# Optimization experiments

Measured on AMD Instinct MI355X. Metric: run time of the kernel, lower is better.

Reference implementation:

```python
import jax, jax.numpy as jnp
import numpy as np

N_SEQ, N_RES, C_M = 512, 256, 256
C_OUTER, C_Z = 32, 128
LN_EPS = 1e-5
NORM_EPS = 1e-3


def setup_inputs() -> dict:
    key = jax.random.key(0)
    ks = jax.random.split(key, 6)
    f32 = jnp.float32
    return {
        "act": jax.random.normal(ks[0], (N_SEQ, N_RES, C_M), f32),
        "mask": jnp.ones((N_SEQ, N_RES), f32),
        # LayerNorm params (create_scale=True, create_offset=True)
        "ln_scale": jnp.ones((C_M,), f32),
        "ln_offset": jnp.zeros((C_M,), f32),
        # left/right projections, 'linear' (VarianceScaling fan_in scale=1)
        "left_w": (jax.random.normal(ks[1], (C_M, C_OUTER), f32) / np.float32(np.sqrt(C_M))),
        "left_b": jnp.zeros((C_OUTER,), f32),
        "right_w": (jax.random.normal(ks[2], (C_M, C_OUTER), f32) / np.float32(np.sqrt(C_M))),
        "right_b": jnp.zeros((C_OUTER,), f32),
        # output_w: VarianceScaling(scale=2.0, fan_in) over (c_outer, c_outer) input dims
        "output_w": (jax.random.normal(ks[3], (C_OUTER, C_OUTER, C_Z), f32)
                     * np.float32(np.sqrt(2.0 / (C_OUTER * C_OUTER)))),
        "output_b": jnp.zeros((C_Z,), f32),
    }


def reference(act, mask, ln_scale, ln_offset, left_w, left_b, right_w, right_b,
              output_w, output_b):
    # LayerNorm over last axis
    mu = jnp.mean(act, axis=-1, keepdims=True)
    var = jnp.var(act, axis=-1, keepdims=True)
    x = (act - mu) * jax.lax.rsqrt(var + LN_EPS) * ln_scale + ln_offset

    m = mask[..., None]  # [N_seq, N_res, 1]
    left = m * (jnp.einsum('abm,mc->abc', x, left_w) + left_b)    # [A,B,Co]
    right = m * (jnp.einsum('abm,me->abe', x, right_w) + right_b)  # [A,D,Co]

    # mean outer product: sum over MSA depth a -> [B, D, Co, Co]
    op = jnp.einsum('abc,ade->bdce', left, right)
    out = jnp.einsum('bdce,cef->bdf', op, output_w) + output_b  # [B, D, Cz]

    # normalization by pairwise mask counts
    norm = jnp.einsum('ab,ad->bd', mask, mask)[..., None]  # [B, D, 1]
    return out / (NORM_EPS + norm)
```

## Files before the change

### kernel.cpp

```cpp
#include <hip/hip_runtime.h>
#include <hip/hip_bf16.h>
#include <stdint.h>

typedef short bf16x8 __attribute__((ext_vector_type(8)));
typedef float f32x4 __attribute__((ext_vector_type(4)));
typedef float f32x16 __attribute__((ext_vector_type(16)));
typedef unsigned short u16x4 __attribute__((ext_vector_type(4)));
typedef unsigned short u16x8 __attribute__((ext_vector_type(8)));

#define GLOAD16(g, l) __builtin_amdgcn_global_load_lds( \
    (const __attribute__((address_space(1))) void*)(g), \
    (__attribute__((address_space(3))) void*)(l), 16, 0, 0)

__device__ __forceinline__ unsigned short f2bf(float f) {
  unsigned u = __float_as_uint(f);
  unsigned r = (u + 0x7fffu + ((u >> 16) & 1u)) >> 16;
  return (unsigned short)r;
}

__global__ __launch_bounds__(256) void prep_norm_k(
    const float* __restrict__ lw, const float* __restrict__ rw,
    const float* __restrict__ ow, const float* __restrict__ mask,
    unsigned short* __restrict__ Wt, unsigned short* __restrict__ wfragG,
    float* __restrict__ nrm) {
  const int bid = blockIdx.x;
  if (bid < 512) {
    int idx = bid * 256 + threadIdx.x;
    if (idx < 131072) {
      int f = idx >> 10, k2 = idx & 1023;
      int e = k2 >> 5, c = k2 & 31;
      Wt[idx] = f2bf(ow[(size_t)((c << 5) + e) * 128 + f]);
    }
    if (idx < 16384) {
      int frag = idx >> 9, lane = (idx >> 3) & 63, j = idx & 7;
      int wc = frag >> 4, ni = (frag >> 3) & 1, kk = frag & 7;
      int mrow = lane & 15, g = lane >> 4;
      int c = wc * 32 + ni * 16 + mrow;
      int k = kk * 32 + g * 8 + j;
      wfragG[idx] = f2bf(c < 32 ? lw[k * 32 + c] : rw[k * 32 + (c - 32)]);
    }
  } else {
    const int b = bid - 512, d = threadIdx.x;
    float s = 0.f;
    #pragma unroll 8
    for (int a = 0; a < 512; ++a)
      s += mask[a * 256 + b] * mask[a * 256 + d];
    nrm[(b << 8) + d] = s;
  }
}

__global__ __launch_bounds__(256, 4) void ln_proj(
    const float* __restrict__ act, const float* __restrict__ mask,
    const float* __restrict__ lns, const float* __restrict__ lno,
    const float* __restrict__ lb, const float* __restrict__ rb,
    const unsigned short* __restrict__ wfragG,
    unsigned short* __restrict__ Lt, unsigned short* __restrict__ Rt) {
  __shared__ char smem[32768];
  const int tid = threadIdx.x;
  const int lane = tid & 63;
  const int w = tid >> 6;
  const int b = blockIdx.y;
  const int a0 = blockIdx.x << 6;
  const int l = tid & 15;
  const int rg = tid >> 4;

  f32x4 sc[4], of[4];
  #pragma unroll
  for (int j = 0; j < 4; ++j) {
    sc[j] = *(const f32x4*)(lns + (l << 4) + (j << 2));
    of[j] = *(const f32x4*)(lno + (l << 4) + (j << 2));
  }

  #pragma unroll
  for (int i = 0; i < 4; ++i) {
    const int r = rg + (i << 4);
    const float* src = act + ((size_t)(a0 + r) * 256 + b) * 256 + (l << 4);
    f32x4 xv[4];
    #pragma unroll
    for (int j = 0; j < 4; ++j) xv[j] = *(const f32x4*)(src + (j << 2));
    float s = 0.f, sq = 0.f;
    #pragma unroll
    for (int j = 0; j < 4; ++j) {
      f32x4 v = xv[j];
      s += v[0] + v[1] + v[2] + v[3];
      sq += v[0] * v[0] + v[1] * v[1] + v[2] * v[2] + v[3] * v[3];
    }
    s += __shfl_xor(s, 1); sq += __shfl_xor(sq, 1);
    s += __shfl_xor(s, 2); sq += __shfl_xor(sq, 2);
    s += __shfl_xor(s, 4); sq += __shfl_xor(sq, 4);
    s += __shfl_xor(s, 8); sq += __shfl_xor(sq, 8);
    const float mu = s * (1.f / 256.f);
    const float rs = rsqrtf(sq * (1.f / 256.f) - mu * mu + 1e-5f);
    #pragma unroll
    for (int hh = 0; hh < 2; ++hh) {
      u16x8 pk;
      #pragma unroll
      for (int j2 = 0; j2 < 2; ++j2) {
        const int j = (hh << 1) + j2;
        #pragma unroll
        for (int e = 0; e < 4; ++e)
          pk[(j2 << 2) + e] = f2bf((xv[j][e] - mu) * rs * sc[j][e] + of[j][e]);
      }
      const int c = (l << 1) + hh;
      *(u16x8*)(smem + (r << 9) + ((c ^ (r & 7)) << 4)) = pk;
    }
  }
  __syncthreads();

  const int wr = w >> 1, wc = w & 1;
  const int mrow = lane & 15, g = lane >> 4;
  f32x4 acc[2][2];
  #pragma unroll
  for (int i = 0; i < 2; ++i)
    #pragma unroll
    for (int jj = 0; jj < 2; ++jj) acc[i][jj] = (f32x4){0.f, 0.f, 0.f, 0.f};
  #pragma unroll
  for (int kk = 0; kk < 8; ++kk) {
    bf16x8 af[2], bfr[2];
    #pragma unroll
    for (int mi = 0; mi < 2; ++mi) {
      const int row = (wr << 5) + (mi << 4) + mrow;
      af[mi] = *(const bf16x8*)(smem + (row << 9) + ((((kk << 2) + g) ^ (row & 7)) << 4));
    }
    #pragma unroll
    for (int ni = 0; ni < 2; ++ni)
      bfr[ni] = *(const bf16x8*)(wfragG + (size_t)((((wc << 1) + ni) << 3) + kk) * 512 + (lane << 3));
    #pragma unroll
    for (int mi = 0; mi < 2; ++mi)
      #pragma unroll
      for (int ni = 0; ni < 2; ++ni)
        acc[mi][ni] = __builtin_amdgcn_mfma_f32_16x16x32_bf16(af[mi], bfr[ni], acc[mi][ni], 0, 0, 0);
  }
  __syncthreads();

  #pragma unroll
  for (int ni = 0; ni < 2; ++ni) {
    const int c = (wc << 5) + (ni << 4) + mrow;
    const float bias = (wc == 0) ? lb[(ni << 4) + mrow] : rb[(ni << 4) + mrow];
    #pragma unroll
    for (int mi = 0; mi < 2; ++mi) {
      const int aB = (wr << 5) + (mi << 4) + (g << 2);
      u16x4 pk;
      #pragma unroll
      for (int qq = 0; qq < 4; ++qq) {
        const float mk = mask[(size_t)(a0 + aB + qq) * 256 + b];
        pk[qq] = f2bf((acc[mi][ni][qq] + bias) * mk);
      }
      *(u16x4*)(smem + (c << 7) + ((((aB >> 3) & 7) ^ (c & 7)) << 4) + ((aB & 7) << 1)) = pk;
    }
  }
  __syncthreads();

  #pragma unroll
  for (int s = 0; s < 2; ++s) {
    const int c = (w << 4) + (s << 3) + (lane >> 3);
    const int gr = lane & 7;
    const u16x8 v = *(const u16x8*)(smem + (c << 7) + ((gr ^ (c & 7)) << 4));
    unsigned short* dst = (c < 32) ? Lt : Rt;
    *(u16x8*)(dst + (size_t)(b * 32 + (c & 31)) * 512 + a0 + (gr << 3)) = v;
  }
}

__global__ __launch_bounds__(512, 2) void gemm_fused(
    const unsigned short* __restrict__ Lt, const unsigned short* __restrict__ Rt,
    const unsigned short* __restrict__ Wt, const float* __restrict__ nrm,
    const float* __restrict__ outb, float* __restrict__ out) {
  __shared__ char smem[131072];
  const int tid = threadIdx.x;
  const int lane = tid & 63;
  const int w = tid >> 6;
  const int wr = w >> 2, wc = w & 3;
  const int l31 = lane & 31, hi = lane >> 5;
  const int mrow = lane & 15, g = lane >> 4;

  const int bid = blockIdx.x;
  const int xcd = bid & 7, jj_ = bid >> 3;
  const int mb = ((jj_ >> 5) << 3) | (jj_ & 7);
  const int nb = (xcd << 2) | ((jj_ >> 3) & 3);
  const int m0i = mb << 8, n0i = nb << 8;

  const int scol = (((tid & 7) ^ ((tid >> 3) & 7)) << 3);

  f32x16 acc32[4][2];
  #pragma unroll
  for (int i = 0; i < 4; ++i)
    #pragma unroll
    for (int jj = 0; jj < 2; ++jj)
      #pragma unroll
      for (int e = 0; e < 16; ++e) acc32[i][jj][e] = 0.f;

  auto STG = [&](const unsigned short* gsrc, int baserow, int dstoff, int kt) {
    GLOAD16(gsrc + ((size_t)(baserow + (tid >> 3)) << 9) + (kt << 6) + scol,
            smem + dstoff + (tid << 4));
  };
  auto STGALL = [&](int buf, int kt) {
    STG(Rt, n0i, buf + 32768, kt);        STG(Rt, n0i + 64, buf + 40960, kt);
    STG(Rt, n0i + 128, buf + 49152, kt);  STG(Rt, n0i + 192, buf + 57344, kt);
    STG(Lt, m0i, buf + 0, kt);            STG(Lt, m0i + 64, buf + 8192, kt);
    STG(Lt, m0i + 128, buf + 16384, kt);  STG(Lt, m0i + 192, buf + 24576, kt);
  };

  STGALL(0, 0);
  STGALL(65536, 1);
  asm volatile("s_waitcnt vmcnt(8)" ::: "memory");
  __builtin_amdgcn_s_barrier();

  #pragma unroll 1
  for (int t = 0; t < 8; ++t) {
    const char* bufp = smem + ((t & 1) << 16);
    #pragma unroll
    for (int kk = 0; kk < 4; ++kk) {
      bf16x8 af[4], bfv[2];
      #pragma unroll
      for (int Mg = 0; Mg < 4; ++Mg) {
        const int row = (wr << 7) + (Mg << 5) + l31;
        af[Mg] = *(const bf16x8*)(bufp + (row << 7) +
                                  ((((kk << 1) + hi) ^ (row & 7)) << 4));
      }
      #pragma unroll
      for (int Ng = 0; Ng < 2; ++Ng) {
        const int row = (wc << 6) + (Ng << 5) + l31;
        bfv[Ng] = *(const bf16x8*)(bufp + 32768 + (row << 7) +
                                   ((((kk << 1) + hi) ^ (row & 7)) << 4));
      }
      #pragma unroll
      for (int Mg = 0; Mg < 4; ++Mg)
        #pragma unroll
        for (int Ng = 0; Ng < 2; ++Ng)
          acc32[Mg][Ng] = __builtin_amdgcn_mfma_f32_32x32x16_bf16(
              af[Mg], bfv[Ng], acc32[Mg][Ng], 0, 0, 0);
    }
    if (t < 6) {
      __builtin_amdgcn_s_barrier();
      STGALL((t & 1) << 16, t + 2);
      asm volatile("s_waitcnt vmcnt(8)" ::: "memory");
      __builtin_amdgcn_s_barrier();
    } else if (t == 6) {
      asm volatile("s_waitcnt vmcnt(0)" ::: "memory");
      __builtin_amdgcn_s_barrier();
    }
  }
  __syncthreads();

  #pragma unroll
  for (int Mg = 0; Mg < 4; ++Mg) {
    #pragma unroll
    for (int Ng = 0; Ng < 2; ++Ng) {
      const int p = (((wr << 2) + Mg) << 3) | ((wc << 1) + Ng);
      #pragma unroll
      for (int q = 0; q < 4; ++q) {
        const int c0 = (q << 3) + (hi << 2);
        const int ow_ = (l31 << 6) + (c0 << 1);
        u16x4 pk;
        #pragma unroll
        for (int j = 0; j < 4; ++j) pk[j] = f2bf(acc32[Mg][Ng][(q << 2) + j]);
        *(u16x4*)(smem + (p << 11) +
                  (ow_ ^ ((p & 7) << 4) ^ (((ow_ >> 7) & 7) << 4))) = pk;
      }
    }
  }
  __syncthreads();

  f32x4 invn[4];
  #pragma unroll
  for (int pg = 0; pg < 4; ++pg) {
    const int bb = (mb << 3) + (pg << 1) + (g >> 1);
    const f32x4 nv = *(const f32x4*)(nrm + (bb << 8) + (nb << 3) + ((g & 1) << 2));
    #pragma unroll
    for (int qq = 0; qq < 4; ++qq) invn[pg][qq] = __builtin_amdgcn_rcpf(1e-3f + nv[qq]);
  }

  const int f0 = w << 4;
  f32x4 acc2[4];
  #pragma unroll
  for (int i = 0; i < 4; ++i) acc2[i] = (f32x4){0.f, 0.f, 0.f, 0.f};
  const unsigned short* wrow = Wt + (size_t)(f0 + mrow) * 1024;
  #pragma unroll 8
  for (int kk2 = 0; kk2 < 32; ++kk2) {
    const bf16x8 b2 = *(const bf16x8*)(wrow + (kk2 << 5) + (g << 3));
    const int orr = (kk2 << 6) + (g << 4);
    #pragma unroll
    for (int pg = 0; pg < 4; ++pg) {
      const int prow = (pg << 4) + mrow;
      const bf16x8 a2 = *(const bf16x8*)(smem + (prow << 11) +
          (orr ^ ((prow & 7) << 4) ^ (((orr >> 7) & 7) << 4)));
      acc2[pg] = __builtin_amdgcn_mfma_f32_16x16x32_bf16(a2, b2, acc2[pg], 0, 0, 0);
    }
  }

  const float ob_ = outb[f0 + mrow];
  #pragma unroll
  for (int pg = 0; pg < 4; ++pg) {
    #pragma unroll
    for (int qq = 0; qq < 4; ++qq) {
      const int p = (pg << 4) + (g << 2) + qq;
      const int bb = (mb << 3) + (p >> 3);
      const int dd = (nb << 3) + (p & 7);
      out[(size_t)((bb << 8) + dd) * 128 + f0 + mrow] = (acc2[pg][qq] + ob_) * invn[pg][qq];
    }
  }
}

extern "C" void kernel_launch(void* const* d_in, const int* in_sizes, int n_in,
                              void* d_out, int out_size, void* d_ws, size_t ws_size,
                              hipStream_t stream) {
  const float* act = (const float*)d_in[0];
  const float* mask = (const float*)d_in[1];
  const float* lns = (const float*)d_in[2];
  const float* lno = (const float*)d_in[3];
  const float* lw = (const float*)d_in[4];
  const float* lb = (const float*)d_in[5];
  const float* rw = (const float*)d_in[6];
  const float* rbv = (const float*)d_in[7];
  const float* ow = (const float*)d_in[8];
  const float* ob = (const float*)d_in[9];
  float* out = (float*)d_out;
  char* ws = (char*)d_ws;

  unsigned short* Lt = (unsigned short*)(ws);
  unsigned short* Rt = (unsigned short*)(ws + 8388608);
  unsigned short* Wt = (unsigned short*)(ws + 16777216);
  unsigned short* wfragG = (unsigned short*)(ws + 17039360);
  float* nrm = (float*)(ws + 17072128);

  hipLaunchKernelGGL(prep_norm_k, dim3(768), dim3(256), 0, stream,
                     lw, rw, ow, mask, Wt, wfragG, nrm);
  hipLaunchKernelGGL(ln_proj, dim3(8, 256), dim3(256), 0, stream,
                     act, mask, lns, lno, lb, rbv, wfragG, Lt, Rt);
  hipLaunchKernelGGL(gemm_fused, dim3(1024), dim3(512), 0, stream,
                     Lt, Rt, Wt, nrm, ob, out);
}
```

Before: 156.7 us.

## Shrink outer-product GEMM tile to 256x128 with triple-buffered 32-wide K pipeline

Rewrites the fused outer-product GEMM to use 256x128 output tiles and 16x16x32 MFMAs instead of 256x256 tiles with 32x32x16 MFMAs. The K loop now runs 16 steps of 32 through a three-stage LDS ring with one barrier per step, and it raises MFMA priority around the compute block. Halving LDS use (73 KB) and accumulator registers lets the kernel target 4 waves per SIMD and launch twice as many blocks, aiming for better latency hiding and load balance. In exchange, A/B reuse per tile drops and global traffic for L rows rises, and the smaller 16x16 MFMAs issue more instructions per FLOP.

```diff
diff --git a/kernel.cpp b/kernel.cpp
--- a/kernel.cpp
+++ b/kernel.cpp
@@ -4,7 +4,6 @@
 
 typedef short bf16x8 __attribute__((ext_vector_type(8)));
 typedef float f32x4 __attribute__((ext_vector_type(4)));
-typedef float f32x16 __attribute__((ext_vector_type(16)));
 typedef unsigned short u16x4 __attribute__((ext_vector_type(4)));
 typedef unsigned short u16x8 __attribute__((ext_vector_type(8)));
 
@@ -161,126 +160,117 @@
   }
 }
 
-__global__ __launch_bounds__(512, 2) void gemm_fused(
+__global__ __launch_bounds__(512, 4) void gemm_fused(
     const unsigned short* __restrict__ Lt, const unsigned short* __restrict__ Rt,
     const unsigned short* __restrict__ Wt, const float* __restrict__ nrm,
     const float* __restrict__ outb, float* __restrict__ out) {
-  __shared__ char smem[131072];
+  __shared__ char smem[73728];
   const int tid = threadIdx.x;
   const int lane = tid & 63;
   const int w = tid >> 6;
-  const int wr = w >> 2, wc = w & 3;
-  const int l31 = lane & 31, hi = lane >> 5;
+  const int wr = w >> 1, wn = w & 1;
   const int mrow = lane & 15, g = lane >> 4;
 
   const int bid = blockIdx.x;
-  const int xcd = bid & 7, jj_ = bid >> 3;
-  const int mb = ((jj_ >> 5) << 3) | (jj_ & 7);
-  const int nb = (xcd << 2) | ((jj_ >> 3) & 3);
-  const int m0i = mb << 8, n0i = nb << 8;
-
-  const int scol = (((tid & 7) ^ ((tid >> 3) & 7)) << 3);
-
-  f32x16 acc32[4][2];
+  const int xcd = bid & 7, j = bid >> 3;
+  const int sub = j & 63;
+  const int mb = ((j >> 6) << 3) + (sub >> 3);
+  const int nb = (xcd << 3) + (sub & 7);
+  const int m0i = mb << 8, n0i = nb << 7;
+
+  const int srow = tid >> 2;
+  const int scol = (((tid & 3) ^ (srow & 3)) << 3);
+
+  f32x4 acc[4][4];
   #pragma unroll
   for (int i = 0; i < 4; ++i)
     #pragma unroll
-    for (int jj = 0; jj < 2; ++jj)
-      #pragma unroll
-      for (int e = 0; e < 16; ++e) acc32[i][jj][e] = 0.f;
-
-  auto STG = [&](const unsigned short* gsrc, int baserow, int dstoff, int kt) {
-    GLOAD16(gsrc + ((size_t)(baserow + (tid >> 3)) << 9) + (kt << 6) + scol,
-            smem + dstoff + (tid << 4));
+    for (int jj = 0; jj < 4; ++jj) acc[i][jj] = (f32x4){0.f, 0.f, 0.f, 0.f};
+
+  auto STGA = [&](int buf, int half, int kt) {
+    GLOAD16(Lt + ((size_t)(m0i + (half << 7) + srow) << 9) + (kt << 5) + scol,
+            smem + buf + (half << 13) + (tid << 4));
   };
-  auto STGALL = [&](int buf, int kt) {
-    STG(Rt, n0i, buf + 32768, kt);        STG(Rt, n0i + 64, buf + 40960, kt);
-    STG(Rt, n0i + 128, buf + 49152, kt);  STG(Rt, n0i + 192, buf + 57344, kt);
-    STG(Lt, m0i, buf + 0, kt);            STG(Lt, m0i + 64, buf + 8192, kt);
-    STG(Lt, m0i + 128, buf + 16384, kt);  STG(Lt, m0i + 192, buf + 24576, kt);
+  auto STGB = [&](int buf, int kt) {
+    GLOAD16(Rt + ((size_t)(n0i + srow) << 9) + (kt << 5) + scol,
+            smem + buf + 16384 + (tid << 4));
   };
 
-  STGALL(0, 0);
-  STGALL(65536, 1);
-  asm volatile("s_waitcnt vmcnt(8)" ::: "memory");
+  STGA(0, 0, 0); STGA(0, 1, 0); STGB(0, 0);
+  STGA(24576, 0, 1); STGA(24576, 1, 1); STGB(24576, 1);
+  asm volatile("s_waitcnt vmcnt(3)" ::: "memory");
   __builtin_amdgcn_s_barrier();
 
+  int cur = 0;
   #pragma unroll 1
-  for (int t = 0; t < 8; ++t) {
-    const char* bufp = smem + ((t & 1) << 16);
-    #pragma unroll
-    for (int kk = 0; kk < 4; ++kk) {
-      bf16x8 af[4], bfv[2];
-      #pragma unroll
-      for (int Mg = 0; Mg < 4; ++Mg) {
-        const int row = (wr << 7) + (Mg << 5) + l31;
-        af[Mg] = *(const bf16x8*)(bufp + (row << 7) +
-                                  ((((kk << 1) + hi) ^ (row & 7)) << 4));
-      }
-      #pragma unroll
-      for (int Ng = 0; Ng < 2; ++Ng) {
-        const int row = (wc << 6) + (Ng << 5) + l31;
-        bfv[Ng] = *(const bf16x8*)(bufp + 32768 + (row << 7) +
-                                   ((((kk << 1) + hi) ^ (row & 7)) << 4));
-      }
-      #pragma unroll
-      for (int Mg = 0; Mg < 4; ++Mg)
-        #pragma unroll
-        for (int Ng = 0; Ng < 2; ++Ng)
-          acc32[Mg][Ng] = __builtin_amdgcn_mfma_f32_32x32x16_bf16(
-              af[Mg], bfv[Ng], acc32[Mg][Ng], 0, 0, 0);
-    }
-    if (t < 6) {
-      __builtin_amdgcn_s_barrier();
-      STGALL((t & 1) << 16, t + 2);
-      asm volatile("s_waitcnt vmcnt(8)" ::: "memory");
-      __builtin_amdgcn_s_barrier();
-    } else if (t == 6) {
-      asm volatile("s_waitcnt vmcnt(0)" ::: "memory");
-      __builtin_amdgcn_s_barrier();
-    }
-  }
-  __syncthreads();
-
-  #pragma unroll
-  for (int Mg = 0; Mg < 4; ++Mg) {
-    #pragma unroll
-    for (int Ng = 0; Ng < 2; ++Ng) {
-      const int p = (((wr << 2) + Mg) << 3) | ((wc << 1) + Ng);
-      #pragma unroll
-      for (int q = 0; q < 4; ++q) {
-        const int c0 = (q << 3) + (hi << 2);
-        const int ow_ = (l31 << 6) + (c0 << 1);
-        u16x4 pk;
-        #pragma unroll
-        for (int j = 0; j < 4; ++j) pk[j] = f2bf(acc32[Mg][Ng][(q << 2) + j]);
-        *(u16x4*)(smem + (p << 11) +
-                  (ow_ ^ ((p & 7) << 4) ^ (((ow_ >> 7) & 7) << 4))) = pk;
-      }
-    }
-  }
-  __syncthreads();
-
-  f32x4 invn[4];
-  #pragma unroll
-  for (int pg = 0; pg < 4; ++pg) {
-    const int bb = (mb << 3) + (pg << 1) + (g >> 1);
-    const f32x4 nv = *(const f32x4*)(nrm + (bb << 8) + (nb << 3) + ((g & 1) << 2));
+  for (int t = 0; t < 16; ++t) {
+    const char* bufp = smem + cur * 24576;
+    bf16x8 af[4], bfv[4];
+    #pragma unroll
+    for (int mi = 0; mi < 4; ++mi) {
+      const int row = (wr << 6) + (mi << 4) + mrow;
+      af[mi] = *(const bf16x8*)(bufp + (row << 6) + ((g ^ (row & 3)) << 4));
+    }
+    #pragma unroll
+    for (int ni = 0; ni < 4; ++ni) {
+      const int row = (wn << 6) + (ni << 4) + mrow;
+      bfv[ni] = *(const bf16x8*)(bufp + 16384 + (row << 6) + ((g ^ (row & 3)) << 4));
+    }
+    if (t < 14) {
+      const int sb = (cur == 0) ? 49152 : (cur == 1) ? 0 : 24576;
+      STGA(sb, 0, t + 2); STGA(sb, 1, t + 2); STGB(sb, t + 2);
+    }
+    asm volatile("s_waitcnt lgkmcnt(0)" ::: "memory");
+    __builtin_amdgcn_sched_barrier(0);
+    __builtin_amdgcn_s_setprio(1);
+    #pragma unroll
+    for (int mi = 0; mi < 4; ++mi)
+      #pragma unroll
+      for (int ni = 0; ni < 4; ++ni)
+        acc[mi][ni] = __builtin_amdgcn_mfma_f32_16x16x32_bf16(
+            af[mi], bfv[ni], acc[mi][ni], 0, 0, 0);
+    __builtin_amdgcn_s_setprio(0);
+    if (t < 14)       asm volatile("s_waitcnt vmcnt(3)" ::: "memory");
+    else if (t == 14) asm volatile("s_waitcnt vmcnt(0)" ::: "memory");
+    __builtin_amdgcn_s_barrier();
+    cur = (cur == 2) ? 0 : cur + 1;
+  }
+  __syncthreads();
+
+  #pragma unroll
+  for (int mi = 0; mi < 4; ++mi) {
+    #pragma unroll
+    for (int ni = 0; ni < 4; ++ni) {
+      const int p = (((wr << 1) + (mi >> 1)) << 2) + (wn << 1) + (ni >> 1);
+      const int ow_ = ((ni & 1) << 10) + (mrow << 6) + ((mi & 1) << 5) + (g << 3);
+      u16x4 pk;
+      #pragma unroll
+      for (int qq = 0; qq < 4; ++qq) pk[qq] = f2bf(acc[mi][ni][qq]);
+      *(u16x4*)(smem + (p << 11) + (ow_ ^ ((p & 7) << 4) ^ (((ow_ >> 7) & 7) << 4))) = pk;
+    }
+  }
+  __syncthreads();
+
+  f32x4 invn[2];
+  #pragma unroll
+  for (int pg = 0; pg < 2; ++pg) {
+    const int bb = (mb << 3) + (pg << 2) + g;
+    const f32x4 nv = *(const f32x4*)(nrm + (bb << 8) + (nb << 2));
     #pragma unroll
     for (int qq = 0; qq < 4; ++qq) invn[pg][qq] = __builtin_amdgcn_rcpf(1e-3f + nv[qq]);
   }
 
   const int f0 = w << 4;
-  f32x4 acc2[4];
-  #pragma unroll
-  for (int i = 0; i < 4; ++i) acc2[i] = (f32x4){0.f, 0.f, 0.f, 0.f};
+  f32x4 acc2[2];
+  acc2[0] = (f32x4){0.f, 0.f, 0.f, 0.f};
+  acc2[1] = (f32x4){0.f, 0.f, 0.f, 0.f};
   const unsigned short* wrow = Wt + (size_t)(f0 + mrow) * 1024;
   #pragma unroll 8
   for (int kk2 = 0; kk2 < 32; ++kk2) {
     const bf16x8 b2 = *(const bf16x8*)(wrow + (kk2 << 5) + (g << 3));
     const int orr = (kk2 << 6) + (g << 4);
     #pragma unroll
-    for (int pg = 0; pg < 4; ++pg) {
+    for (int pg = 0; pg < 2; ++pg) {
       const int prow = (pg << 4) + mrow;
       const bf16x8 a2 = *(const bf16x8*)(smem + (prow << 11) +
           (orr ^ ((prow & 7) << 4) ^ (((orr >> 7) & 7) << 4)));
@@ -290,12 +280,12 @@
 
   const float ob_ = outb[f0 + mrow];
   #pragma unroll
-  for (int pg = 0; pg < 4; ++pg) {
+  for (int pg = 0; pg < 2; ++pg) {
     #pragma unroll
     for (int qq = 0; qq < 4; ++qq) {
       const int p = (pg << 4) + (g << 2) + qq;
-      const int bb = (mb << 3) + (p >> 3);
-      const int dd = (nb << 3) + (p & 7);
+      const int bb = (mb << 3) + (p >> 2);
+      const int dd = (nb << 2) + (p & 3);
       out[(size_t)((bb << 8) + dd) * 128 + f0 + mrow] = (acc2[pg][qq] + ob_) * invn[pg][qq];
     }
   }
@@ -327,6 +317,6 @@
                      lw, rw, ow, mask, Wt, wfragG, nrm);
   hipLaunchKernelGGL(ln_proj, dim3(8, 256), dim3(256), 0, stream,
                      act, mask, lns, lno, lb, rbv, wfragG, Lt, Rt);
-  hipLaunchKernelGGL(gemm_fused, dim3(1024), dim3(512), 0, stream,
+  hipLaunchKernelGGL(gemm_fused, dim3(2048), dim3(512), 0, stream,
                      Lt, Rt, Wt, nrm, ob, out);
 }
```

Result: slower. 184.5 us (+17.7%).
